# Optimization experiments

Hardware: AMD Instinct MI355X
Metric: run time of the kernel (lower is better)

Reference implementation:

```python
import jax, jax.numpy as jnp
import numpy as np

B, T, E, H = 8, 1024, 1024, 16
D = E // H  # per-head dim = 64


def setup_inputs() -> dict:
    key = jax.random.key(0)
    ks = jax.random.split(key, 10)
    s = 0.05
    return {
        "source": jax.random.normal(ks[0], (B, T, E), jnp.float32),
        "target": jax.random.normal(ks[1], (B, T, E), jnp.float32),
        "W_q": jax.random.normal(ks[2], (1, H, D, D), jnp.float32) * s,
        "W_v": jax.random.normal(ks[3], (1, H, D, D), jnp.float32) * s,
        "W_o": jax.random.normal(ks[4], (1, H, D, D), jnp.float32) * s,
        "W_ih": jax.random.normal(ks[5], (H, D, D), jnp.float32) * s,
        "W_hh": jax.random.normal(ks[6], (H, D, D), jnp.float32) * s,
        "b_ih": jax.random.normal(ks[7], (H, D), jnp.float32) * s,
        "b_hh": jax.random.normal(ks[8], (H, D), jnp.float32) * s,
    }


def reference(source, target, W_q, W_v, W_o, W_ih, W_hh, b_ih, b_hh):
    b, t, e = source.shape
    h = W_ih.shape[0]
    d = e // h
    # split heads: [B, H, T, d]
    q = source.reshape(b, t, h, d).transpose(0, 2, 1, 3)
    k = target.reshape(b, t, h, d).transpose(0, 2, 1, 3)
    v = k
    # per-head projections (grammar path: k is NOT projected)
    q = jnp.einsum('bhtd,hde->bhte', q, W_q[0])
    v = jnp.einsum('bhtd,hde->bhte', v, W_v[0])
    # RNN positional key generation (per head, batch_first nn.RNN, tanh).
    # step 0: input = k[:, :, 0, :], hidden = 0  ->  h1 = tanh(x @ Wih^T + b_ih + b_hh)
    k0 = k[:, :, 0, :]  # [B, H, d]
    h1 = jnp.tanh(jnp.einsum('bhd,hed->bhe', k0, W_ih) + b_ih + b_hh)
    # steps t>=1: next_word fed back as BOTH input and hidden state
    def step(hs, _):
        hn = jnp.tanh(jnp.einsum('bhd,hed->bhe', hs, W_ih) + b_ih
                      + jnp.einsum('bhd,hed->bhe', hs, W_hh) + b_hh)
        return hn, hn
    _, rest = jax.lax.scan(step, h1, None, length=t - 1)  # [T-1, B, H, d]
    nw = jnp.concatenate([h1[None], rest], axis=0).transpose(1, 2, 0, 3)  # [B,H,T,d]
    # scores / sqrt(d)  (time_attention), then merge_attn divides by sqrt(T)
    scores = jnp.einsum('bhqd,bhkd->bhqk', q, nw) / float(np.sqrt(d))
    w = jax.nn.softmax(scores / float(np.sqrt(t)), axis=-1)
    out = jnp.einsum('bhqk,bhkd->bhqd', w, v)
    out = jnp.einsum('bhtd,hde->bhte', out, W_o[0])
    return out.transpose(0, 2, 1, 3).reshape(b, t, e)
```

## Files before the change

kernel.cpp:

```cpp
#include <hip/hip_runtime.h>

typedef unsigned short u16;
typedef short short8 __attribute__((ext_vector_type(8)));
typedef float f32x4 __attribute__((ext_vector_type(4)));
typedef _Float16 f16;
typedef f16 f16x2 __attribute__((ext_vector_type(2)));
typedef f16 f16x8 __attribute__((ext_vector_type(8)));

#define B_ 8
#define T_ 1024
#define E_ 1024
#define H_ 16
#define D_ 64
#define BH_ 128

__device__ __forceinline__ float ftanh(float x){
    x = fminf(8.0f, fmaxf(-8.0f, x));
    float e2 = __expf(2.0f * x);
    return 1.0f - 2.0f * __builtin_amdgcn_rcpf(e2 + 1.0f);
}

__device__ __forceinline__ u16 f2h(float x){
    union { f16 h; u16 u; } v; v.h = (f16)x; return v.u;
}

__device__ __forceinline__ float dot8(f16x8 a, f16x8 b, float acc){
#if __has_builtin(__builtin_amdgcn_fdot2)
    f16x2 a0 = {a[0],a[1]}, a1 = {a[2],a[3]}, a2 = {a[4],a[5]}, a3 = {a[6],a[7]};
    f16x2 b0 = {b[0],b[1]}, b1 = {b[2],b[3]}, b2 = {b[4],b[5]}, b3 = {b[6],b[7]};
    acc = __builtin_amdgcn_fdot2(a0, b0, acc, false);
    acc = __builtin_amdgcn_fdot2(a1, b1, acc, false);
    acc = __builtin_amdgcn_fdot2(a2, b2, acc, false);
    acc = __builtin_amdgcn_fdot2(a3, b3, acc, false);
#else
    #pragma unroll
    for (int i = 0; i < 8; ++i) acc += (float)a[i] * (float)b[i];
#endif
    return acc;
}

__device__ __forceinline__ f16x8 pack8(f32x4 a, f32x4 b){
    f16x8 r;
    r[0]=(f16)a[0]; r[1]=(f16)a[1]; r[2]=(f16)a[2]; r[3]=(f16)a[3];
    r[4]=(f16)b[0]; r[5]=(f16)b[1]; r[6]=(f16)b[2]; r[7]=(f16)b[3];
    return r;
}

#define PIN8(x) do { f32x4 _t = __builtin_bit_cast(f32x4, x); \
                     asm volatile("" : "+v"(_t));             \
                     x = __builtin_bit_cast(f16x8, _t); } while (0)

__global__ __launch_bounds__(256, 1) void proj_rnn_kernel(
    const float* __restrict__ src, const float* __restrict__ tgt,
    const float* __restrict__ Wq,  const float* __restrict__ Wv,
    const float* __restrict__ Wih, const float* __restrict__ Whh,
    const float* __restrict__ bih, const float* __restrict__ bhh,
    u16* __restrict__ qh, u16* __restrict__ vh, u16* __restrict__ nwh)
{
    int bid = blockIdx.x;
    if (bid < BH_) {
        if (threadIdx.x >= 64) return;
        __shared__ __align__(16) u16 hl[D_];
        const int b = bid >> 4, h = bid & 15;
        const int e = threadIdx.x;

        const f32x4* wi4 = (const f32x4*)(Wih + ((size_t)h * D_ + e) * D_);
        const f32x4* wh4 = (const f32x4*)(Whh + ((size_t)h * D_ + e) * D_);
        float c = bih[h * D_ + e] + bhh[h * D_ + e];
        asm volatile("" : "+v"(c));

        f16x8 n0 = pack8(wi4[0],  wi4[1]),  n1 = pack8(wi4[2],  wi4[3]);
        f16x8 n2 = pack8(wi4[4],  wi4[5]),  n3 = pack8(wi4[6],  wi4[7]);
        f16x8 n4 = pack8(wi4[8],  wi4[9]),  n5 = pack8(wi4[10], wi4[11]);
        f16x8 n6 = pack8(wi4[12], wi4[13]), n7 = pack8(wi4[14], wi4[15]);
        f16x8 m0 = pack8(wi4[0]+wh4[0],   wi4[1]+wh4[1]);
        f16x8 m1 = pack8(wi4[2]+wh4[2],   wi4[3]+wh4[3]);
        f16x8 m2 = pack8(wi4[4]+wh4[4],   wi4[5]+wh4[5]);
        f16x8 m3 = pack8(wi4[6]+wh4[6],   wi4[7]+wh4[7]);
        f16x8 m4 = pack8(wi4[8]+wh4[8],   wi4[9]+wh4[9]);
        f16x8 m5 = pack8(wi4[10]+wh4[10], wi4[11]+wh4[11]);
        f16x8 m6 = pack8(wi4[12]+wh4[12], wi4[13]+wh4[13]);
        f16x8 m7 = pack8(wi4[14]+wh4[14], wi4[15]+wh4[15]);
        PIN8(m0); PIN8(m1); PIN8(m2); PIN8(m3);
        PIN8(m4); PIN8(m5); PIN8(m6); PIN8(m7);

        hl[e] = f2h(tgt[(size_t)b * T_ * E_ + h * D_ + e]);

        u16* nwp = nwh + (size_t)bid * T_ * D_;
        const f16x8* hl8 = (const f16x8*)hl;

        {
            f16x8 x0=hl8[0],x1=hl8[1],x2=hl8[2],x3=hl8[3],
                  x4=hl8[4],x5=hl8[5],x6=hl8[6],x7=hl8[7];
            float s0=dot8(n0,x0,c),   s1=dot8(n1,x1,0.f),
                  s2=dot8(n2,x2,0.f), s3=dot8(n3,x3,0.f),
                  s4=dot8(n4,x4,0.f), s5=dot8(n5,x5,0.f),
                  s6=dot8(n6,x6,0.f), s7=dot8(n7,x7,0.f);
            float hv = ftanh(((s0+s1)+(s2+s3)) + ((s4+s5)+(s6+s7)));
            u16 hb = f2h(hv);
            hl[e] = hb;
            nwp[e] = hb;
        }

        #pragma unroll 1
        for (int t = 1; t < T_; ++t) {
            f16x8 x0=hl8[0],x1=hl8[1],x2=hl8[2],x3=hl8[3],
                  x4=hl8[4],x5=hl8[5],x6=hl8[6],x7=hl8[7];
            float s0=dot8(m0,x0,c),   s1=dot8(m1,x1,0.f),
                  s2=dot8(m2,x2,0.f), s3=dot8(m3,x3,0.f),
                  s4=dot8(m4,x4,0.f), s5=dot8(m5,x5,0.f),
                  s6=dot8(m6,x6,0.f), s7=dot8(m7,x7,0.f);
            float hv = ftanh(((s0+s1)+(s2+s3)) + ((s4+s5)+(s6+s7)));
            u16 hb = f2h(hv);
            hl[e] = hb;
            nwp[(size_t)t * D_ + e] = hb;
        }
    } else {
        int pb   = bid - BH_;
        int bh   = pb >> 5;
        int tile = pb & 31;
        int b = bh >> 4, h = bh & 15;
        int e  = threadIdx.x & 63;
        int tg = threadIdx.x >> 6;
        int t0 = tile * 32 + tg * 8;

        const float* wq = Wq + (size_t)h * D_ * D_ + e;
        const float* wv = Wv + (size_t)h * D_ * D_ + e;
        const float* s0 = src + ((size_t)b * T_ + t0) * E_ + h * D_;
        const float* g0 = tgt + ((size_t)b * T_ + t0) * E_ + h * D_;

        float aq[8] = {0,0,0,0,0,0,0,0};
        float av[8] = {0,0,0,0,0,0,0,0};
        #pragma unroll 4
        for (int d4 = 0; d4 < 16; ++d4) {
            float q0 = wq[(4*d4+0)*64], q1 = wq[(4*d4+1)*64],
                  q2 = wq[(4*d4+2)*64], q3 = wq[(4*d4+3)*64];
            float v0 = wv[(4*d4+0)*64], v1 = wv[(4*d4+1)*64],
                  v2 = wv[(4*d4+2)*64], v3 = wv[(4*d4+3)*64];
            #pragma unroll
            for (int j = 0; j < 8; ++j) {
                float4 x = *(const float4*)(s0 + (size_t)j * E_ + 4*d4);
                float4 y = *(const float4*)(g0 + (size_t)j * E_ + 4*d4);
                aq[j] += x.x*q0 + x.y*q1 + x.z*q2 + x.w*q3;
                av[j] += y.x*v0 + y.y*v1 + y.z*v2 + y.w*v3;
            }
        }
        u16* qp = qh + ((size_t)bh * T_ + t0) * D_ + e;
        #pragma unroll
        for (int j = 0; j < 8; ++j) qp[(size_t)j * D_] = f2h(aq[j] * (1.0f/256.0f));
        f16x8 vv;
        #pragma unroll
        for (int j = 0; j < 8; ++j) vv[j] = (f16)av[j];
        *(f16x8*)(vh + ((size_t)bh * D_ + e) * T_ + t0) = vv;
    }
}

#define MFMA16(a, b, c) __builtin_amdgcn_mfma_f32_16x16x32_f16(a, b, c, 0, 0, 0)

__global__ __launch_bounds__(256) void attn_kernel(
    const u16* __restrict__ qh,
    const u16* __restrict__ kh,
    const u16* __restrict__ vh,
    const float* __restrict__ Wo,
    float* __restrict__ out)
{
    __shared__ __align__(16) u16 Klds[64 * 64];
    __shared__ __align__(16) u16 Vlds[64 * 64];
    __shared__ __align__(16) u16 Plds[4][2][16 * 64];

    const int tid  = threadIdx.x;
    const int lane = tid & 63;
    const int w    = tid >> 6;
    const int l15  = lane & 15;
    const int quad = lane >> 4;
    const int sw   = lane & 7;
    const int bh   = blockIdx.y;
    const int qt   = blockIdx.x;

    const size_t base  = (size_t)bh * T_ * D_;
    const size_t vbase = (size_t)bh * D_ * T_;

    f16x8 aq[2][2];
    #pragma unroll
    for (int g = 0; g < 2; ++g) {
        int qrow = qt * 128 + (w + 4 * g) * 16 + l15;
        const f16x8* qp = (const f16x8*)(qh + base + (size_t)qrow * 64 + quad * 8);
        aq[g][0] = qp[0];
        aq[g][1] = qp[4];
    }

    f32x4 oacc[2][4];
    float lrun[2][4];
    #pragma unroll
    for (int g = 0; g < 2; ++g)
        #pragma unroll
        for (int i = 0; i < 4; ++i) {
            oacc[g][i] = (f32x4){0.f, 0.f, 0.f, 0.f};
            lrun[g][i] = 0.f;
        }

    #pragma unroll 1
    for (int kt = 0; kt < 16; ++kt) {
        #pragma unroll
        for (int i = 0; i < 2; ++i) {
            int ch = tid + 256 * i;
            int r = ch >> 3, cc = ch & 7;
            short8 kval = *(const short8*)(kh + base + (size_t)(kt * 64 + r) * 64 + cc * 8);
            *(short8*)&Klds[r * 64 + ((cc ^ (r & 7)) * 8)] = kval;
            short8 vval = *(const short8*)(vh + vbase + (size_t)r * T_ + kt * 64 + cc * 8);
            *(short8*)&Vlds[r * 64 + ((cc ^ (r & 7)) * 8)] = vval;
        }
        __syncthreads();

        f32x4 sacc[2][4];
        #pragma unroll
        for (int u = 0; u < 4; ++u) {
            int row = 16 * u + l15;
            f16x8 bk0 = *(const f16x8*)&Klds[row * 64 + (((quad + 0) ^ sw) * 8)];
            f16x8 bk1 = *(const f16x8*)&Klds[row * 64 + (((quad + 4) ^ sw) * 8)];
            #pragma unroll
            for (int g = 0; g < 2; ++g) {
                f32x4 z = (f32x4){0.f, 0.f, 0.f, 0.f};
                z = MFMA16(aq[g][0], bk0, z);
                z = MFMA16(aq[g][1], bk1, z);
                sacc[g][u] = z;
            }
        }

        #pragma unroll
        for (int g = 0; g < 2; ++g) {
            float pr[4][4];
            #pragma unroll
            for (int r = 0; r < 4; ++r) {
                float rs = 0.f;
                #pragma unroll
                for (int u = 0; u < 4; ++u) {
                    float pv = __expf(sacc[g][u][r]);
                    pr[u][r] = pv;
                    rs += pv;
                }
                lrun[g][r] += rs;
            }
            u16* Pw = Plds[w][g];
            #pragma unroll
            for (int u = 0; u < 4; ++u) {
                int col = 16 * u + l15;
                #pragma unroll
                for (int r = 0; r < 4; ++r) {
                    int row = quad * 4 + r;
                    Pw[row * 64 + (((col >> 3) ^ (row & 7)) * 8) + (col & 7)] = f2h(pr[u][r]);
                }
            }
        }

        #pragma unroll
        for (int kc = 0; kc < 2; ++kc) {
            int csel = ((quad + 4 * kc) ^ sw) * 8;
            f16x8 ap0 = *(const f16x8*)&Plds[w][0][l15 * 64 + csel];
            f16x8 ap1 = *(const f16x8*)&Plds[w][1][l15 * 64 + csel];
            #pragma unroll
            for (int nt = 0; nt < 4; ++nt) {
                f16x8 bv = *(const f16x8*)&Vlds[(16 * nt + l15) * 64 + csel];
                oacc[0][nt] = MFMA16(ap0, bv, oacc[0][nt]);
                oacc[1][nt] = MFMA16(ap1, bv, oacc[1][nt]);
            }
        }
        __syncthreads();
    }

    float inv[2][4];
    #pragma unroll
    for (int g = 0; g < 2; ++g)
        #pragma unroll
        for (int r = 0; r < 4; ++r) {
            float s = lrun[g][r];
            #pragma unroll
            for (int off = 1; off < 16; off <<= 1)
                s += __shfl_xor(s, off, 16);
            inv[g][r] = __builtin_amdgcn_rcpf(s);
        }

    const int b  = bh >> 4, hh = bh & 15;
    {
        const float* wo = Wo + (size_t)hh * D_ * D_;
        #pragma unroll
        for (int i = 0; i < 2; ++i) {
            int ch = tid + 256 * i;
            int e = ch >> 3, dc = ch & 7;
            short8 vch;
            #pragma unroll
            for (int j = 0; j < 8; ++j)
                vch[j] = (short)f2h(wo[(size_t)(dc * 8 + j) * D_ + e]);
            *(short8*)&Klds[e * 64 + ((dc ^ (e & 7)) * 8)] = vch;
        }
    }
    #pragma unroll
    for (int g = 0; g < 2; ++g) {
        u16* Pw = Plds[w][g];
        #pragma unroll
        for (int nt = 0; nt < 4; ++nt) {
            int col = 16 * nt + l15;
            #pragma unroll
            for (int r = 0; r < 4; ++r) {
                int row = quad * 4 + r;
                Pw[row * 64 + (((col >> 3) ^ (row & 7)) * 8) + (col & 7)] =
                    f2h(oacc[g][nt][r] * inv[g][r]);
            }
        }
    }
    __syncthreads();

    f16x8 ao[2][2];
    #pragma unroll
    for (int g = 0; g < 2; ++g) {
        ao[g][0] = *(const f16x8*)&Plds[w][g][l15 * 64 + (((quad + 0) ^ sw) * 8)];
        ao[g][1] = *(const f16x8*)&Plds[w][g][l15 * 64 + (((quad + 4) ^ sw) * 8)];
    }
    f32x4 oo[2][4];
    #pragma unroll
    for (int g = 0; g < 2; ++g)
        #pragma unroll
        for (int nt = 0; nt < 4; ++nt)
            oo[g][nt] = (f32x4){0.f, 0.f, 0.f, 0.f};
    #pragma unroll
    for (int nt = 0; nt < 4; ++nt) {
        int erow = 16 * nt + l15;
        f16x8 b0 = *(const f16x8*)&Klds[erow * 64 + (((quad + 0) ^ (erow & 7)) * 8)];
        f16x8 b1 = *(const f16x8*)&Klds[erow * 64 + (((quad + 4) ^ (erow & 7)) * 8)];
        #pragma unroll
        for (int g = 0; g < 2; ++g) {
            oo[g][nt] = MFMA16(ao[g][0], b0, oo[g][nt]);
            oo[g][nt] = MFMA16(ao[g][1], b1, oo[g][nt]);
        }
    }
    #pragma unroll
    for (int g = 0; g < 2; ++g)
        #pragma unroll
        for (int nt = 0; nt < 4; ++nt)
            #pragma unroll
            for (int r = 0; r < 4; ++r) {
                int qg = qt * 128 + (w + 4 * g) * 16 + quad * 4 + r;
                int e  = 16 * nt + l15;
                out[((size_t)b * T_ + qg) * E_ + hh * D_ + e] = oo[g][nt][r];
            }
}

extern "C" void kernel_launch(void* const* d_in, const int* in_sizes, int n_in,
                              void* d_out, int out_size, void* d_ws, size_t ws_size,
                              hipStream_t stream)
{
    const float* src = (const float*)d_in[0];
    const float* tgt = (const float*)d_in[1];
    const float* Wq  = (const float*)d_in[2];
    const float* Wv  = (const float*)d_in[3];
    const float* Wo  = (const float*)d_in[4];
    const float* Wih = (const float*)d_in[5];
    const float* Whh = (const float*)d_in[6];
    const float* bih = (const float*)d_in[7];
    const float* bhh = (const float*)d_in[8];
    float* out = (float*)d_out;

    char* ws = (char*)d_ws;
    u16* qh  = (u16*)(ws);
    u16* vh  = (u16*)(ws + (size_t)16 * 1024 * 1024);
    u16* nwh = (u16*)(ws + (size_t)32 * 1024 * 1024);

    (void)in_sizes; (void)n_in; (void)out_size; (void)ws_size;

    proj_rnn_kernel<<<dim3(BH_ + 4096), 256, 0, stream>>>(
        src, tgt, Wq, Wv, Wih, Whh, bih, bhh, qh, vh, nwh);
    attn_kernel<<<dim3(8, BH_), 256, 0, stream>>>(qh, nwh, vh, Wo, out);
}
```

Before: 374.5 us.

## Compute RNN recurrence matvec with MFMA instead of per-lane fdot2 chains

Replaces each lane's 64-element dot product, built from a chain of fdot2 calls, with eight 16x16x32 MFMA instructions that compute the full 64x64 weight-by-hidden product. Each lane then picks its output element through a select tree and writes it to LDS at a permuted row index. The aim is to shorten the latency of each serial recurrence step, which sits on the critical path across 1024 timesteps. In exchange it adds MFMA latency and a dependency chain of two MFMAs plus selects per step, and most of each MFMA's output is discarded because only one column of the hidden-state operand is meaningful.

```diff
diff --git a/kernel.cpp b/kernel.cpp
--- a/kernel.cpp
+++ b/kernel.cpp
@@ -24,21 +24,6 @@
     union { f16 h; u16 u; } v; v.h = (f16)x; return v.u;
 }
 
-__device__ __forceinline__ float dot8(f16x8 a, f16x8 b, float acc){
-#if __has_builtin(__builtin_amdgcn_fdot2)
-    f16x2 a0 = {a[0],a[1]}, a1 = {a[2],a[3]}, a2 = {a[4],a[5]}, a3 = {a[6],a[7]};
-    f16x2 b0 = {b[0],b[1]}, b1 = {b[2],b[3]}, b2 = {b[4],b[5]}, b3 = {b[6],b[7]};
-    acc = __builtin_amdgcn_fdot2(a0, b0, acc, false);
-    acc = __builtin_amdgcn_fdot2(a1, b1, acc, false);
-    acc = __builtin_amdgcn_fdot2(a2, b2, acc, false);
-    acc = __builtin_amdgcn_fdot2(a3, b3, acc, false);
-#else
-    #pragma unroll
-    for (int i = 0; i < 8; ++i) acc += (float)a[i] * (float)b[i];
-#endif
-    return acc;
-}
-
 __device__ __forceinline__ f16x8 pack8(f32x4 a, f32x4 b){
     f16x8 r;
     r[0]=(f16)a[0]; r[1]=(f16)a[1]; r[2]=(f16)a[2]; r[3]=(f16)a[3];
@@ -49,6 +34,9 @@
 #define PIN8(x) do { f32x4 _t = __builtin_bit_cast(f32x4, x); \
                      asm volatile("" : "+v"(_t));             \
                      x = __builtin_bit_cast(f16x8, _t); } while (0)
+#define PIN4(x) do { asm volatile("" : "+v"(x)); } while (0)
+
+#define MFMA16(a, b, c) __builtin_amdgcn_mfma_f32_16x16x32_f16(a, b, c, 0, 0, 0)
 
 __global__ __launch_bounds__(256, 1) void proj_rnn_kernel(
     const float* __restrict__ src, const float* __restrict__ tgt,
@@ -62,59 +50,80 @@
         if (threadIdx.x >= 64) return;
         __shared__ __align__(16) u16 hl[D_];
         const int b = bid >> 4, h = bid & 15;
-        const int e = threadIdx.x;
-
-        const f32x4* wi4 = (const f32x4*)(Wih + ((size_t)h * D_ + e) * D_);
-        const f32x4* wh4 = (const f32x4*)(Whh + ((size_t)h * D_ + e) * D_);
-        float c = bih[h * D_ + e] + bhh[h * D_ + e];
-        asm volatile("" : "+v"(c));
-
-        f16x8 n0 = pack8(wi4[0],  wi4[1]),  n1 = pack8(wi4[2],  wi4[3]);
-        f16x8 n2 = pack8(wi4[4],  wi4[5]),  n3 = pack8(wi4[6],  wi4[7]);
-        f16x8 n4 = pack8(wi4[8],  wi4[9]),  n5 = pack8(wi4[10], wi4[11]);
-        f16x8 n6 = pack8(wi4[12], wi4[13]), n7 = pack8(wi4[14], wi4[15]);
-        f16x8 m0 = pack8(wi4[0]+wh4[0],   wi4[1]+wh4[1]);
-        f16x8 m1 = pack8(wi4[2]+wh4[2],   wi4[3]+wh4[3]);
-        f16x8 m2 = pack8(wi4[4]+wh4[4],   wi4[5]+wh4[5]);
-        f16x8 m3 = pack8(wi4[6]+wh4[6],   wi4[7]+wh4[7]);
-        f16x8 m4 = pack8(wi4[8]+wh4[8],   wi4[9]+wh4[9]);
-        f16x8 m5 = pack8(wi4[10]+wh4[10], wi4[11]+wh4[11]);
-        f16x8 m6 = pack8(wi4[12]+wh4[12], wi4[13]+wh4[13]);
-        f16x8 m7 = pack8(wi4[14]+wh4[14], wi4[15]+wh4[15]);
-        PIN8(m0); PIN8(m1); PIN8(m2); PIN8(m3);
-        PIN8(m4); PIN8(m5); PIN8(m6); PIN8(m7);
-
-        hl[e] = f2h(tgt[(size_t)b * T_ * E_ + h * D_ + e]);
+        const int l    = threadIdx.x;
+        const int l15  = l & 15;
+        const int quad = l >> 4;
+        const int rsel = 16 * (l & 3) + 4 * quad + ((l >> 2) & 3);
+        const bool b0 = (l & 1), b1 = (l & 2), b2 = (l & 4), b3 = (l & 8);
+
+        const float* WI = Wih + (size_t)h * D_ * D_;
+        const float* WH = Whh + (size_t)h * D_ * D_;
+        f16x8 n00,n01,n10,n11,n20,n21,n30,n31;
+        f16x8 m00,m01,m10,m11,m20,m21,m30,m31;
+        {
+            #define LOADF(rb, kb, NV, MV) do {                                    \
+                const float* pI = WI + (size_t)(16*(rb) + l15) * D_ + quad*8 + 32*(kb); \
+                const float* pH = WH + (size_t)(16*(rb) + l15) * D_ + quad*8 + 32*(kb); \
+                f32x4 ia = *(const f32x4*)pI, ib = *(const f32x4*)(pI + 4);       \
+                f32x4 ha = *(const f32x4*)pH, hb = *(const f32x4*)(pH + 4);       \
+                NV = pack8(ia, ib);                                               \
+                MV = pack8(ia + ha, ib + hb);                                     \
+            } while (0)
+            LOADF(0,0,n00,m00); LOADF(0,1,n01,m01);
+            LOADF(1,0,n10,m10); LOADF(1,1,n11,m11);
+            LOADF(2,0,n20,m20); LOADF(2,1,n21,m21);
+            LOADF(3,0,n30,m30); LOADF(3,1,n31,m31);
+            #undef LOADF
+        }
+        f32x4 cb0, cb1, cb2, cb3;
+        {
+            const float* bi = bih + h * D_;
+            const float* bh2 = bhh + h * D_;
+            #pragma unroll
+            for (int i = 0; i < 4; ++i) {
+                cb0[i] = bi[ 0 + 4*quad + i] + bh2[ 0 + 4*quad + i];
+                cb1[i] = bi[16 + 4*quad + i] + bh2[16 + 4*quad + i];
+                cb2[i] = bi[32 + 4*quad + i] + bh2[32 + 4*quad + i];
+                cb3[i] = bi[48 + 4*quad + i] + bh2[48 + 4*quad + i];
+            }
+        }
+        PIN8(m00); PIN8(m01); PIN8(m10); PIN8(m11);
+        PIN8(m20); PIN8(m21); PIN8(m30); PIN8(m31);
+        PIN4(cb0); PIN4(cb1); PIN4(cb2); PIN4(cb3);
+
+        hl[l] = f2h(tgt[(size_t)b * T_ * E_ + h * D_ + l]);
 
         u16* nwp = nwh + (size_t)bid * T_ * D_;
-        const f16x8* hl8 = (const f16x8*)hl;
-
-        {
-            f16x8 x0=hl8[0],x1=hl8[1],x2=hl8[2],x3=hl8[3],
-                  x4=hl8[4],x5=hl8[5],x6=hl8[6],x7=hl8[7];
-            float s0=dot8(n0,x0,c),   s1=dot8(n1,x1,0.f),
-                  s2=dot8(n2,x2,0.f), s3=dot8(n3,x3,0.f),
-                  s4=dot8(n4,x4,0.f), s5=dot8(n5,x5,0.f),
-                  s6=dot8(n6,x6,0.f), s7=dot8(n7,x7,0.f);
-            float hv = ftanh(((s0+s1)+(s2+s3)) + ((s4+s5)+(s6+s7)));
-            u16 hb = f2h(hv);
-            hl[e] = hb;
-            nwp[e] = hb;
-        }
+
+        #define RNN_STEP(A00,A01,A10,A11,A20,A21,A30,A31, trow) do {             \
+            f16x8 hb0 = *(const f16x8*)(hl + quad * 8);                          \
+            f16x8 hb1 = *(const f16x8*)(hl + 32 + quad * 8);                     \
+            f32x4 a0 = MFMA16(A00, hb0, cb0);                                    \
+            f32x4 a1 = MFMA16(A10, hb0, cb1);                                    \
+            f32x4 a2 = MFMA16(A20, hb0, cb2);                                    \
+            f32x4 a3 = MFMA16(A30, hb0, cb3);                                    \
+            a0 = MFMA16(A01, hb1, a0);                                           \
+            a1 = MFMA16(A11, hb1, a1);                                           \
+            a2 = MFMA16(A21, hb1, a2);                                           \
+            a3 = MFMA16(A31, hb1, a3);                                           \
+            f32x4 t0 = b0 ? a1 : a0;                                             \
+            f32x4 t1 = b0 ? a3 : a2;                                             \
+            f32x4 z  = b1 ? t1 : t0;                                             \
+            float u0 = b2 ? z[1] : z[0];                                         \
+            float u1 = b2 ? z[3] : z[2];                                         \
+            float yv = b3 ? u1 : u0;                                             \
+            u16 hb16 = f2h(ftanh(yv));                                           \
+            hl[rsel] = hb16;                                                     \
+            nwp[(size_t)(trow) * D_ + rsel] = hb16;                              \
+        } while (0)
+
+        RNN_STEP(n00,n01,n10,n11,n20,n21,n30,n31, 0);
 
         #pragma unroll 1
         for (int t = 1; t < T_; ++t) {
-            f16x8 x0=hl8[0],x1=hl8[1],x2=hl8[2],x3=hl8[3],
-                  x4=hl8[4],x5=hl8[5],x6=hl8[6],x7=hl8[7];
-            float s0=dot8(m0,x0,c),   s1=dot8(m1,x1,0.f),
-                  s2=dot8(m2,x2,0.f), s3=dot8(m3,x3,0.f),
-                  s4=dot8(m4,x4,0.f), s5=dot8(m5,x5,0.f),
-                  s6=dot8(m6,x6,0.f), s7=dot8(m7,x7,0.f);
-            float hv = ftanh(((s0+s1)+(s2+s3)) + ((s4+s5)+(s6+s7)));
-            u16 hb = f2h(hv);
-            hl[e] = hb;
-            nwp[(size_t)t * D_ + e] = hb;
-        }
+            RNN_STEP(m00,m01,m10,m11,m20,m21,m30,m31, t);
+        }
+        #undef RNN_STEP
     } else {
         int pb   = bid - BH_;
         int bh   = pb >> 5;
@@ -154,8 +163,6 @@
         *(f16x8*)(vh + ((size_t)bh * D_ + e) * T_ + t0) = vv;
     }
 }
-
-#define MFMA16(a, b, c) __builtin_amdgcn_mfma_f32_16x16x32_f16(a, b, c, 0, 0, 0)
 
 __global__ __launch_bounds__(256) void attn_kernel(
     const u16* __restrict__ qh,
```

Result: slower. 460.7 us (+23.0%).

## Keep softmax P in registers via permlane swaps instead of LDS round-trip

Applied to the files above, without the earlier changes.

The score MFMA now computes the transposed product (K as A operand, Q as B operand), so each lane holds scores for one query column. Exponentials are packed to fp16 with cvt_pkrtz, and the PV A-fragment is rebuilt in registers with v_permlane16/32_swap, removing the per-tile write and read of P through LDS. Row sums are reduced with two cross-lane shuffles and broadcast back afterward. A runtime probe checks the permlane semantics at kernel start and falls back to __shfl_xor if they do not match, which roughly doubles code size and adds some select logic.

```diff
diff --git a/kernel.cpp b/kernel.cpp
--- a/kernel.cpp
+++ b/kernel.cpp
@@ -1,6 +1,7 @@
 #include <hip/hip_runtime.h>
 
 typedef unsigned short u16;
+typedef unsigned int   u32;
 typedef short short8 __attribute__((ext_vector_type(8)));
 typedef float f32x4 __attribute__((ext_vector_type(4)));
 typedef _Float16 f16;
@@ -49,6 +50,8 @@
 #define PIN8(x) do { f32x4 _t = __builtin_bit_cast(f32x4, x); \
                      asm volatile("" : "+v"(_t));             \
                      x = __builtin_bit_cast(f16x8, _t); } while (0)
+
+#define MFMA16(a, b, c) __builtin_amdgcn_mfma_f32_16x16x32_f16(a, b, c, 0, 0, 0)
 
 __global__ __launch_bounds__(256, 1) void proj_rnn_kernel(
     const float* __restrict__ src, const float* __restrict__ tgt,
@@ -155,7 +158,193 @@
     }
 }
 
-#define MFMA16(a, b, c) __builtin_amdgcn_mfma_f32_16x16x32_f16(a, b, c, 0, 0, 0)
+union U4 { u32 u[4]; f16x8 v; };
+
+template<bool UP>
+__device__ __forceinline__ u32 ex16(u32 x, bool sel){
+    if (UP) {
+        u32 a = x, b = x;
+        asm volatile("v_permlane16_swap_b32 %0, %1" : "+v"(a), "+v"(b));
+        return sel ? a : b;
+    }
+    return (u32)__shfl_xor((int)x, 16);
+}
+template<bool UP>
+__device__ __forceinline__ u32 ex32(u32 x, bool sel){
+    if (UP) {
+        u32 a = x, b = x;
+        asm volatile("v_permlane32_swap_b32 %0, %1" : "+v"(a), "+v"(b));
+        return sel ? a : b;
+    }
+    return (u32)__shfl_xor((int)x, 32);
+}
+
+template<bool UP>
+__device__ __forceinline__ f16x8 build_afrag(u32 A0, u32 A1, u32 B0, u32 B1,
+                                             bool b4, bool b5, bool sel16, bool sel32){
+    u32 Z0 = b5 ? B0 : A0, Z1 = b5 ? B1 : A1;
+    u32 W0 = b5 ? A0 : B0, W1 = b5 ? A1 : B1;
+    u32 xZ0 = ex16<UP>(Z0, sel16), xZ1 = ex16<UP>(Z1, sel16);
+    u32 V0  = ex32<UP>(W0, sel32), V1  = ex32<UP>(W1, sel32);
+    u32 X0  = ex16<UP>(V0, sel16), X1  = ex16<UP>(V1, sel16);
+    U4 r;
+    r.u[0] = b5 ? (b4 ? xZ0 : V0) : (b4 ? X0 : Z0);
+    r.u[1] = b5 ? (b4 ? xZ1 : V1) : (b4 ? X1 : Z1);
+    r.u[2] = b5 ? (b4 ? Z0 : X0) : (b4 ? V0 : xZ0);
+    r.u[3] = b5 ? (b4 ? Z1 : X1) : (b4 ? V1 : xZ1);
+    return r.v;
+}
+
+__device__ __forceinline__ u32 pkrtz(float a, float b){
+    return __builtin_bit_cast(u32, __builtin_amdgcn_cvt_pkrtz(a, b));
+}
+
+template<bool UP>
+__device__ __forceinline__ void attn_core(
+    const u16* __restrict__ kh, const u16* __restrict__ vh,
+    const float* __restrict__ Wo, float* __restrict__ out,
+    u16* Klds, u16* Vlds, u16* PldsW,
+    size_t base, size_t vbase,
+    int tid, int w, int l15, int quad, int sw,
+    int bh, int qt, bool b4m, bool b5m, bool sel16, bool sel32,
+    const f16x8 (&aq)[2][2])
+{
+    f32x4 oacc[2][4];
+    float lrun[2] = {0.f, 0.f};
+    #pragma unroll
+    for (int g = 0; g < 2; ++g)
+        #pragma unroll
+        for (int i = 0; i < 4; ++i)
+            oacc[g][i] = (f32x4){0.f, 0.f, 0.f, 0.f};
+
+    #pragma unroll 1
+    for (int kt = 0; kt < 16; ++kt) {
+        #pragma unroll
+        for (int i = 0; i < 2; ++i) {
+            int ch = tid + 256 * i;
+            int r = ch >> 3, cc = ch & 7;
+            short8 kval = *(const short8*)(kh + base + (size_t)(kt * 64 + r) * 64 + cc * 8);
+            *(short8*)&Klds[r * 64 + ((cc ^ (r & 7)) * 8)] = kval;
+            short8 vval = *(const short8*)(vh + vbase + (size_t)r * T_ + kt * 64 + cc * 8);
+            *(short8*)&Vlds[r * 64 + ((cc ^ (r & 7)) * 8)] = vval;
+        }
+        __syncthreads();
+
+        u32 pk[2][4][2];
+        #pragma unroll
+        for (int u = 0; u < 4; ++u) {
+            int row = 16 * u + l15;
+            f16x8 bk0 = *(const f16x8*)&Klds[row * 64 + (((quad + 0) ^ sw) * 8)];
+            f16x8 bk1 = *(const f16x8*)&Klds[row * 64 + (((quad + 4) ^ sw) * 8)];
+            #pragma unroll
+            for (int g = 0; g < 2; ++g) {
+                f32x4 z = (f32x4){0.f, 0.f, 0.f, 0.f};
+                z = MFMA16(bk0, aq[g][0], z);
+                z = MFMA16(bk1, aq[g][1], z);
+                float e0 = __expf(z[0]), e1 = __expf(z[1]);
+                float e2 = __expf(z[2]), e3 = __expf(z[3]);
+                lrun[g] += (e0 + e1) + (e2 + e3);
+                pk[g][u][0] = pkrtz(e0, e1);
+                pk[g][u][1] = pkrtz(e2, e3);
+            }
+        }
+
+        #pragma unroll
+        for (int kc = 0; kc < 2; ++kc) {
+            f16x8 ap0 = build_afrag<UP>(pk[0][2*kc][0], pk[0][2*kc][1],
+                                        pk[0][2*kc+1][0], pk[0][2*kc+1][1],
+                                        b4m, b5m, sel16, sel32);
+            f16x8 ap1 = build_afrag<UP>(pk[1][2*kc][0], pk[1][2*kc][1],
+                                        pk[1][2*kc+1][0], pk[1][2*kc+1][1],
+                                        b4m, b5m, sel16, sel32);
+            int csel = ((quad + 4 * kc) ^ sw) * 8;
+            #pragma unroll
+            for (int nt = 0; nt < 4; ++nt) {
+                f16x8 bv = *(const f16x8*)&Vlds[(16 * nt + l15) * 64 + csel];
+                oacc[0][nt] = MFMA16(ap0, bv, oacc[0][nt]);
+                oacc[1][nt] = MFMA16(ap1, bv, oacc[1][nt]);
+            }
+        }
+        __syncthreads();
+    }
+
+    float invr[2][4];
+    #pragma unroll
+    for (int g = 0; g < 2; ++g) {
+        float s = lrun[g];
+        s += __shfl_xor(s, 16);
+        s += __shfl_xor(s, 32);
+        float iv = __builtin_amdgcn_rcpf(s);
+        #pragma unroll
+        for (int r = 0; r < 4; ++r)
+            invr[g][r] = __shfl(iv, quad * 4 + r, 16);
+    }
+
+    const int b  = bh >> 4, hh = bh & 15;
+    {
+        const float* wo = Wo + (size_t)hh * D_ * D_;
+        #pragma unroll
+        for (int i = 0; i < 2; ++i) {
+            int ch = tid + 256 * i;
+            int e = ch >> 3, dc = ch & 7;
+            short8 vch;
+            #pragma unroll
+            for (int j = 0; j < 8; ++j)
+                vch[j] = (short)f2h(wo[(size_t)(dc * 8 + j) * D_ + e]);
+            *(short8*)&Klds[e * 64 + ((dc ^ (e & 7)) * 8)] = vch;
+        }
+    }
+    #pragma unroll
+    for (int g = 0; g < 2; ++g) {
+        u16* Pw = PldsW + g * 16 * 64;
+        #pragma unroll
+        for (int nt = 0; nt < 4; ++nt) {
+            int col = 16 * nt + l15;
+            #pragma unroll
+            for (int r = 0; r < 4; ++r) {
+                int row = quad * 4 + r;
+                Pw[row * 64 + (((col >> 3) ^ (row & 7)) * 8) + (col & 7)] =
+                    f2h(oacc[g][nt][r] * invr[g][r]);
+            }
+        }
+    }
+    __syncthreads();
+
+    f16x8 ao[2][2];
+    #pragma unroll
+    for (int g = 0; g < 2; ++g) {
+        const u16* Pw = PldsW + g * 16 * 64;
+        ao[g][0] = *(const f16x8*)&Pw[l15 * 64 + (((quad + 0) ^ sw) * 8)];
+        ao[g][1] = *(const f16x8*)&Pw[l15 * 64 + (((quad + 4) ^ sw) * 8)];
+    }
+    f32x4 oo[2][4];
+    #pragma unroll
+    for (int g = 0; g < 2; ++g)
+        #pragma unroll
+        for (int nt = 0; nt < 4; ++nt)
+            oo[g][nt] = (f32x4){0.f, 0.f, 0.f, 0.f};
+    #pragma unroll
+    for (int nt = 0; nt < 4; ++nt) {
+        int erow = 16 * nt + l15;
+        f16x8 b0 = *(const f16x8*)&Klds[erow * 64 + (((quad + 0) ^ (erow & 7)) * 8)];
+        f16x8 b1 = *(const f16x8*)&Klds[erow * 64 + (((quad + 4) ^ (erow & 7)) * 8)];
+        #pragma unroll
+        for (int g = 0; g < 2; ++g) {
+            oo[g][nt] = MFMA16(ao[g][0], b0, oo[g][nt]);
+            oo[g][nt] = MFMA16(ao[g][1], b1, oo[g][nt]);
+        }
+    }
+    #pragma unroll
+    for (int g = 0; g < 2; ++g)
+        #pragma unroll
+        for (int nt = 0; nt < 4; ++nt)
+            #pragma unroll
+            for (int r = 0; r < 4; ++r) {
+                int qg = qt * 128 + (w + 4 * g) * 16 + quad * 4 + r;
+                int e  = 16 * nt + l15;
+                out[((size_t)b * T_ + qg) * E_ + hh * D_ + e] = oo[g][nt][r];
+            }
+}
 
 __global__ __launch_bounds__(256) void attn_kernel(
     const u16* __restrict__ qh,
@@ -176,9 +365,21 @@
     const int sw   = lane & 7;
     const int bh   = blockIdx.y;
     const int qt   = blockIdx.x;
+    const bool b4m = (quad & 1) != 0;
+    const bool b5m = quad >= 2;
 
     const size_t base  = (size_t)bh * T_ * D_;
     const size_t vbase = (size_t)bh * D_ * T_;
+
+    u32 cx = (u32)lane, cy = (u32)lane;
+    asm volatile("v_permlane16_swap_b32 %0, %1" : "+v"(cx), "+v"(cy));
+    const bool sel16 = (cx == (u32)(lane ^ 16));
+    const bool ok16  = sel16 || (cy == (u32)(lane ^ 16));
+    u32 dx = (u32)lane, dy = (u32)lane;
+    asm volatile("v_permlane32_swap_b32 %0, %1" : "+v"(dx), "+v"(dy));
+    const bool sel32 = (dx == (u32)(lane ^ 32));
+    const bool ok32  = sel32 || (dy == (u32)(lane ^ 32));
+    const bool ok    = __all(ok16 && ok32);
 
     f16x8 aq[2][2];
     #pragma unroll
@@ -189,160 +390,14 @@
         aq[g][1] = qp[4];
     }
 
-    f32x4 oacc[2][4];
-    float lrun[2][4];
-    #pragma unroll
-    for (int g = 0; g < 2; ++g)
-        #pragma unroll
-        for (int i = 0; i < 4; ++i) {
-            oacc[g][i] = (f32x4){0.f, 0.f, 0.f, 0.f};
-            lrun[g][i] = 0.f;
-        }
-
-    #pragma unroll 1
-    for (int kt = 0; kt < 16; ++kt) {
-        #pragma unroll
-        for (int i = 0; i < 2; ++i) {
-            int ch = tid + 256 * i;
-            int r = ch >> 3, cc = ch & 7;
-            short8 kval = *(const short8*)(kh + base + (size_t)(kt * 64 + r) * 64 + cc * 8);
-            *(short8*)&Klds[r * 64 + ((cc ^ (r & 7)) * 8)] = kval;
-            short8 vval = *(const short8*)(vh + vbase + (size_t)r * T_ + kt * 64 + cc * 8);
-            *(short8*)&Vlds[r * 64 + ((cc ^ (r & 7)) * 8)] = vval;
-        }
-        __syncthreads();
-
-        f32x4 sacc[2][4];
-        #pragma unroll
-        for (int u = 0; u < 4; ++u) {
-            int row = 16 * u + l15;
-            f16x8 bk0 = *(const f16x8*)&Klds[row * 64 + (((quad + 0) ^ sw) * 8)];
-            f16x8 bk1 = *(const f16x8*)&Klds[row * 64 + (((quad + 4) ^ sw) * 8)];
-            #pragma unroll
-            for (int g = 0; g < 2; ++g) {
-                f32x4 z = (f32x4){0.f, 0.f, 0.f, 0.f};
-                z = MFMA16(aq[g][0], bk0, z);
-                z = MFMA16(aq[g][1], bk1, z);
-                sacc[g][u] = z;
-            }
-        }
-
-        #pragma unroll
-        for (int g = 0; g < 2; ++g) {
-            float pr[4][4];
-            #pragma unroll
-            for (int r = 0; r < 4; ++r) {
-                float rs = 0.f;
-                #pragma unroll
-                for (int u = 0; u < 4; ++u) {
-                    float pv = __expf(sacc[g][u][r]);
-                    pr[u][r] = pv;
-                    rs += pv;
-                }
-                lrun[g][r] += rs;
-            }
-            u16* Pw = Plds[w][g];
-            #pragma unroll
-            for (int u = 0; u < 4; ++u) {
-                int col = 16 * u + l15;
-                #pragma unroll
-                for (int r = 0; r < 4; ++r) {
-                    int row = quad * 4 + r;
-                    Pw[row * 64 + (((col >> 3) ^ (row & 7)) * 8) + (col & 7)] = f2h(pr[u][r]);
-                }
-            }
-        }
-
-        #pragma unroll
-        for (int kc = 0; kc < 2; ++kc) {
-            int csel = ((quad + 4 * kc) ^ sw) * 8;
-            f16x8 ap0 = *(const f16x8*)&Plds[w][0][l15 * 64 + csel];
-            f16x8 ap1 = *(const f16x8*)&Plds[w][1][l15 * 64 + csel];
-            #pragma unroll
-            for (int nt = 0; nt < 4; ++nt) {
-                f16x8 bv = *(const f16x8*)&Vlds[(16 * nt + l15) * 64 + csel];
-                oacc[0][nt] = MFMA16(ap0, bv, oacc[0][nt]);
-                oacc[1][nt] = MFMA16(ap1, bv, oacc[1][nt]);
-            }
-        }
-        __syncthreads();
-    }
-
-    float inv[2][4];
-    #pragma unroll
-    for (int g = 0; g < 2; ++g)
-        #pragma unroll
-        for (int r = 0; r < 4; ++r) {
-            float s = lrun[g][r];
-            #pragma unroll
-            for (int off = 1; off < 16; off <<= 1)
-                s += __shfl_xor(s, off, 16);
-            inv[g][r] = __builtin_amdgcn_rcpf(s);
-        }
-
-    const int b  = bh >> 4, hh = bh & 15;
-    {
-        const float* wo = Wo + (size_t)hh * D_ * D_;
-        #pragma unroll
-        for (int i = 0; i < 2; ++i) {
-            int ch = tid + 256 * i;
-            int e = ch >> 3, dc = ch & 7;
-            short8 vch;
-            #pragma unroll
-            for (int j = 0; j < 8; ++j)
-                vch[j] = (short)f2h(wo[(size_t)(dc * 8 + j) * D_ + e]);
-            *(short8*)&Klds[e * 64 + ((dc ^ (e & 7)) * 8)] = vch;
-        }
-    }
-    #pragma unroll
-    for (int g = 0; g < 2; ++g) {
-        u16* Pw = Plds[w][g];
-        #pragma unroll
-        for (int nt = 0; nt < 4; ++nt) {
-            int col = 16 * nt + l15;
-            #pragma unroll
-            for (int r = 0; r < 4; ++r) {
-                int row = quad * 4 + r;
-                Pw[row * 64 + (((col >> 3) ^ (row & 7)) * 8) + (col & 7)] =
-                    f2h(oacc[g][nt][r] * inv[g][r]);
-            }
-        }
-    }
-    __syncthreads();
-
-    f16x8 ao[2][2];
-    #pragma unroll
-    for (int g = 0; g < 2; ++g) {
-        ao[g][0] = *(const f16x8*)&Plds[w][g][l15 * 64 + (((quad + 0) ^ sw) * 8)];
-        ao[g][1] = *(const f16x8*)&Plds[w][g][l15 * 64 + (((quad + 4) ^ sw) * 8)];
-    }
-    f32x4 oo[2][4];
-    #pragma unroll
-    for (int g = 0; g < 2; ++g)
-        #pragma unroll
-        for (int nt = 0; nt < 4; ++nt)
-            oo[g][nt] = (f32x4){0.f, 0.f, 0.f, 0.f};
-    #pragma unroll
-    for (int nt = 0; nt < 4; ++nt) {
-        int erow = 16 * nt + l15;
-        f16x8 b0 = *(const f16x8*)&Klds[erow * 64 + (((quad + 0) ^ (erow & 7)) * 8)];
-        f16x8 b1 = *(const f16x8*)&Klds[erow * 64 + (((quad + 4) ^ (erow & 7)) * 8)];
-        #pragma unroll
-        for (int g = 0; g < 2; ++g) {
-            oo[g][nt] = MFMA16(ao[g][0], b0, oo[g][nt]);
-            oo[g][nt] = MFMA16(ao[g][1], b1, oo[g][nt]);
-        }
-    }
-    #pragma unroll
-    for (int g = 0; g < 2; ++g)
-        #pragma unroll
-        for (int nt = 0; nt < 4; ++nt)
-            #pragma unroll
-            for (int r = 0; r < 4; ++r) {
-                int qg = qt * 128 + (w + 4 * g) * 16 + quad * 4 + r;
-                int e  = 16 * nt + l15;
-                out[((size_t)b * T_ + qg) * E_ + hh * D_ + e] = oo[g][nt][r];
-            }
+    if (ok)
+        attn_core<true >(kh, vh, Wo, out, Klds, Vlds, &Plds[w][0][0],
+                         base, vbase, tid, w, l15, quad, sw,
+                         bh, qt, b4m, b5m, sel16, sel32, aq);
+    else
+        attn_core<false>(kh, vh, Wo, out, Klds, Vlds, &Plds[w][0][0],
+                         base, vbase, tid, w, l15, quad, sw,
+                         bh, qt, b4m, b5m, sel16, sel32, aq);
 }
 
 extern "C" void kernel_launch(void* const* d_in, const int* in_sizes, int n_in,
```

Measured after the change: 392.3 us. +4.8%, slower.

## Double-buffer K/V tiles in attention and swap grid dimension order

Applied to the files above, without the earlier changes.

The attention kernel now register-prefetches the next K/V tile while computing on the current one. The prefetched tile is stored into a second LDS buffer, which cuts one barrier per iteration. The P staging buffer shrinks to one per wave because each q-group's PV MFMAs now run right after its softmax. The grid axes are swapped so consecutive blocks cover different heads. This costs more LDS and more registers for the prefetch, and L2 locality changes.

```diff
diff --git a/kernel.cpp b/kernel.cpp
--- a/kernel.cpp
+++ b/kernel.cpp
@@ -49,6 +49,8 @@
 #define PIN8(x) do { f32x4 _t = __builtin_bit_cast(f32x4, x); \
                      asm volatile("" : "+v"(_t));             \
                      x = __builtin_bit_cast(f16x8, _t); } while (0)
+
+#define MFMA16(a, b, c) __builtin_amdgcn_mfma_f32_16x16x32_f16(a, b, c, 0, 0, 0)
 
 __global__ __launch_bounds__(256, 1) void proj_rnn_kernel(
     const float* __restrict__ src, const float* __restrict__ tgt,
@@ -155,8 +157,6 @@
     }
 }
 
-#define MFMA16(a, b, c) __builtin_amdgcn_mfma_f32_16x16x32_f16(a, b, c, 0, 0, 0)
-
 __global__ __launch_bounds__(256) void attn_kernel(
     const u16* __restrict__ qh,
     const u16* __restrict__ kh,
@@ -164,9 +164,9 @@
     const float* __restrict__ Wo,
     float* __restrict__ out)
 {
-    __shared__ __align__(16) u16 Klds[64 * 64];
-    __shared__ __align__(16) u16 Vlds[64 * 64];
-    __shared__ __align__(16) u16 Plds[4][2][16 * 64];
+    __shared__ __align__(16) u16 Klds[2][64 * 64];
+    __shared__ __align__(16) u16 Vlds[2][64 * 64];
+    __shared__ __align__(16) u16 Plds[4][16 * 64];
 
     const int tid  = threadIdx.x;
     const int lane = tid & 63;
@@ -174,8 +174,8 @@
     const int l15  = lane & 15;
     const int quad = lane >> 4;
     const int sw   = lane & 7;
-    const int bh   = blockIdx.y;
-    const int qt   = blockIdx.x;
+    const int bh   = blockIdx.x;
+    const int qt   = blockIdx.y;
 
     const size_t base  = (size_t)bh * T_ * D_;
     const size_t vbase = (size_t)bh * D_ * T_;
@@ -199,25 +199,41 @@
             lrun[g][i] = 0.f;
         }
 
+    #pragma unroll
+    for (int i = 0; i < 2; ++i) {
+        int ch = tid + 256 * i;
+        int r = ch >> 3, cc = ch & 7;
+        short8 kval = *(const short8*)(kh + base + (size_t)r * 64 + cc * 8);
+        *(short8*)&Klds[0][r * 64 + ((cc ^ (r & 7)) * 8)] = kval;
+        short8 vval = *(const short8*)(vh + vbase + (size_t)r * T_ + cc * 8);
+        *(short8*)&Vlds[0][r * 64 + ((cc ^ (r & 7)) * 8)] = vval;
+    }
+    __syncthreads();
+
     #pragma unroll 1
     for (int kt = 0; kt < 16; ++kt) {
-        #pragma unroll
-        for (int i = 0; i < 2; ++i) {
-            int ch = tid + 256 * i;
-            int r = ch >> 3, cc = ch & 7;
-            short8 kval = *(const short8*)(kh + base + (size_t)(kt * 64 + r) * 64 + cc * 8);
-            *(short8*)&Klds[r * 64 + ((cc ^ (r & 7)) * 8)] = kval;
-            short8 vval = *(const short8*)(vh + vbase + (size_t)r * T_ + kt * 64 + cc * 8);
-            *(short8*)&Vlds[r * 64 + ((cc ^ (r & 7)) * 8)] = vval;
-        }
-        __syncthreads();
+        const int cur = kt & 1;
+
+        short8 kpre[2], vpre[2];
+        if (kt < 15) {
+            #pragma unroll
+            for (int i = 0; i < 2; ++i) {
+                int ch = tid + 256 * i;
+                int r = ch >> 3, cc = ch & 7;
+                kpre[i] = *(const short8*)(kh + base + (size_t)((kt + 1) * 64 + r) * 64 + cc * 8);
+                vpre[i] = *(const short8*)(vh + vbase + (size_t)r * T_ + (kt + 1) * 64 + cc * 8);
+            }
+        }
+
+        const u16* Kb = Klds[cur];
+        const u16* Vb = Vlds[cur];
 
         f32x4 sacc[2][4];
         #pragma unroll
         for (int u = 0; u < 4; ++u) {
             int row = 16 * u + l15;
-            f16x8 bk0 = *(const f16x8*)&Klds[row * 64 + (((quad + 0) ^ sw) * 8)];
-            f16x8 bk1 = *(const f16x8*)&Klds[row * 64 + (((quad + 4) ^ sw) * 8)];
+            f16x8 bk0 = *(const f16x8*)&Kb[row * 64 + (((quad + 0) ^ sw) * 8)];
+            f16x8 bk1 = *(const f16x8*)&Kb[row * 64 + (((quad + 4) ^ sw) * 8)];
             #pragma unroll
             for (int g = 0; g < 2; ++g) {
                 f32x4 z = (f32x4){0.f, 0.f, 0.f, 0.f};
@@ -241,7 +257,7 @@
                 }
                 lrun[g][r] += rs;
             }
-            u16* Pw = Plds[w][g];
+            u16* Pw = Plds[w];
             #pragma unroll
             for (int u = 0; u < 4; ++u) {
                 int col = 16 * u + l15;
@@ -251,18 +267,26 @@
                     Pw[row * 64 + (((col >> 3) ^ (row & 7)) * 8) + (col & 7)] = f2h(pr[u][r]);
                 }
             }
-        }
-
-        #pragma unroll
-        for (int kc = 0; kc < 2; ++kc) {
-            int csel = ((quad + 4 * kc) ^ sw) * 8;
-            f16x8 ap0 = *(const f16x8*)&Plds[w][0][l15 * 64 + csel];
-            f16x8 ap1 = *(const f16x8*)&Plds[w][1][l15 * 64 + csel];
-            #pragma unroll
-            for (int nt = 0; nt < 4; ++nt) {
-                f16x8 bv = *(const f16x8*)&Vlds[(16 * nt + l15) * 64 + csel];
-                oacc[0][nt] = MFMA16(ap0, bv, oacc[0][nt]);
-                oacc[1][nt] = MFMA16(ap1, bv, oacc[1][nt]);
+            #pragma unroll
+            for (int kc = 0; kc < 2; ++kc) {
+                int csel = ((quad + 4 * kc) ^ sw) * 8;
+                f16x8 ap = *(const f16x8*)&Pw[l15 * 64 + csel];
+                #pragma unroll
+                for (int nt = 0; nt < 4; ++nt) {
+                    f16x8 bv = *(const f16x8*)&Vb[(16 * nt + l15) * 64 + csel];
+                    oacc[g][nt] = MFMA16(ap, bv, oacc[g][nt]);
+                }
+            }
+        }
+
+        if (kt < 15) {
+            const int nxt = cur ^ 1;
+            #pragma unroll
+            for (int i = 0; i < 2; ++i) {
+                int ch = tid + 256 * i;
+                int r = ch >> 3, cc = ch & 7;
+                *(short8*)&Klds[nxt][r * 64 + ((cc ^ (r & 7)) * 8)] = kpre[i];
+                *(short8*)&Vlds[nxt][r * 64 + ((cc ^ (r & 7)) * 8)] = vpre[i];
             }
         }
         __syncthreads();
@@ -291,31 +315,30 @@
             #pragma unroll
             for (int j = 0; j < 8; ++j)
                 vch[j] = (short)f2h(wo[(size_t)(dc * 8 + j) * D_ + e]);
-            *(short8*)&Klds[e * 64 + ((dc ^ (e & 7)) * 8)] = vch;
-        }
-    }
-    #pragma unroll
-    for (int g = 0; g < 2; ++g) {
-        u16* Pw = Plds[w][g];
-        #pragma unroll
-        for (int nt = 0; nt < 4; ++nt) {
-            int col = 16 * nt + l15;
-            #pragma unroll
-            for (int r = 0; r < 4; ++r) {
-                int row = quad * 4 + r;
-                Pw[row * 64 + (((col >> 3) ^ (row & 7)) * 8) + (col & 7)] =
-                    f2h(oacc[g][nt][r] * inv[g][r]);
-            }
+            *(short8*)&Klds[0][e * 64 + ((dc ^ (e & 7)) * 8)] = vch;
+        }
+    }
+    f16x8 ao[2][2];
+    {
+        u16* Pw = Plds[w];
+        #pragma unroll
+        for (int g = 0; g < 2; ++g) {
+            #pragma unroll
+            for (int nt = 0; nt < 4; ++nt) {
+                int col = 16 * nt + l15;
+                #pragma unroll
+                for (int r = 0; r < 4; ++r) {
+                    int row = quad * 4 + r;
+                    Pw[row * 64 + (((col >> 3) ^ (row & 7)) * 8) + (col & 7)] =
+                        f2h(oacc[g][nt][r] * inv[g][r]);
+                }
+            }
+            ao[g][0] = *(const f16x8*)&Pw[l15 * 64 + (((quad + 0) ^ sw) * 8)];
+            ao[g][1] = *(const f16x8*)&Pw[l15 * 64 + (((quad + 4) ^ sw) * 8)];
         }
     }
     __syncthreads();
 
-    f16x8 ao[2][2];
-    #pragma unroll
-    for (int g = 0; g < 2; ++g) {
-        ao[g][0] = *(const f16x8*)&Plds[w][g][l15 * 64 + (((quad + 0) ^ sw) * 8)];
-        ao[g][1] = *(const f16x8*)&Plds[w][g][l15 * 64 + (((quad + 4) ^ sw) * 8)];
-    }
     f32x4 oo[2][4];
     #pragma unroll
     for (int g = 0; g < 2; ++g)
@@ -325,8 +348,8 @@
     #pragma unroll
     for (int nt = 0; nt < 4; ++nt) {
         int erow = 16 * nt + l15;
-        f16x8 b0 = *(const f16x8*)&Klds[erow * 64 + (((quad + 0) ^ (erow & 7)) * 8)];
-        f16x8 b1 = *(const f16x8*)&Klds[erow * 64 + (((quad + 4) ^ (erow & 7)) * 8)];
+        f16x8 b0 = *(const f16x8*)&Klds[0][erow * 64 + (((quad + 0) ^ (erow & 7)) * 8)];
+        f16x8 b1 = *(const f16x8*)&Klds[0][erow * 64 + (((quad + 4) ^ (erow & 7)) * 8)];
         #pragma unroll
         for (int g = 0; g < 2; ++g) {
             oo[g][nt] = MFMA16(ao[g][0], b0, oo[g][nt]);
@@ -369,5 +392,5 @@
 
     proj_rnn_kernel<<<dim3(BH_ + 4096), 256, 0, stream>>>(
         src, tgt, Wq, Wv, Wih, Whh, bih, bhh, qh, vh, nwh);
-    attn_kernel<<<dim3(8, BH_), 256, 0, stream>>>(qh, nwh, vh, Wo, out);
-}
+    attn_kernel<<<dim3(BH_, 8), 256, 0, stream>>>(qh, nwh, vh, Wo, out);
+}
```

Result: faster. 365.3 us (-2.5%).
